# Kernel optimization log

Hardware: AMD Instinct MI355X
Metric: run time of the kernel (lower is better)

## Reference

```python
import jax, jax.numpy as jnp
import numpy as np

DIM = 192
T, H, W = 6, 8, 8
NH = 6
HD = DIM // NH
HW = H * W
N = T * HW
SCALE = HD ** (-0.5)
B_ = 128


def _sine_pos_enc():
    # Faithful port of get_sine_position_encoding(window_size[1:], dim // 2).
    npf = DIM // 2
    ones = jnp.ones((1, H, W), jnp.float32)
    y_embed = jnp.cumsum(ones, axis=1)
    x_embed = jnp.cumsum(ones, axis=2)
    two_pi = 2.0 * np.pi
    y_embed = y_embed / (y_embed[:, -1:, :] + 1e-6) * two_pi
    x_embed = x_embed / (x_embed[:, :, -1:] + 1e-6) * two_pi
    dim_t = jnp.arange(npf, dtype=jnp.float32)
    dim_t = 10000.0 ** (2.0 * jnp.floor(dim_t / 2.0) / npf)
    pos_x = x_embed[:, :, :, None] / dim_t
    pos_y = y_embed[:, :, :, None] / dim_t
    pos_x = jnp.stack((jnp.sin(pos_x[..., 0::2]), jnp.cos(pos_x[..., 1::2])), axis=4).reshape(1, H, W, npf)
    pos_y = jnp.stack((jnp.sin(pos_y[..., 0::2]), jnp.cos(pos_y[..., 1::2])), axis=4).reshape(1, H, W, npf)
    pos = jnp.concatenate((pos_y, pos_x), axis=3)  # (1, H, W, DIM)
    return pos.reshape(1, HW, DIM)


def setup_inputs() -> dict:
    key = jax.random.key(0)
    ks = jax.random.split(key, 6)
    s = 0.02
    return {
        "x": jax.random.normal(ks[0], (B_, N, DIM), jnp.float32),
        "Wqkv": jax.random.normal(ks[1], (3 * DIM, DIM), jnp.float32) * s,
        "Wproj": jax.random.normal(ks[2], (DIM, 2 * DIM), jnp.float32) * s,
        "bproj": jnp.zeros((DIM,), jnp.float32),
        "gamma": jnp.ones((DIM,), jnp.float32),
        "beta": jnp.zeros((DIM,), jnp.float32),
        "W1": jax.random.normal(ks[3], (DIM, DIM), jnp.float32) * s,
        "b1": jnp.zeros((DIM,), jnp.float32),
        "W2": jax.random.normal(ks[4], (DIM, DIM), jnp.float32) * s,
        "b2": jnp.zeros((DIM,), jnp.float32),
    }


def reference(x, Wqkv, Wproj, bproj, gamma, beta, W1, b1, W2, b2):
    b = x.shape[0]
    pos = jnp.tile(_sine_pos_enc(), (1, T, 1))  # (1, N, DIM)
    qkv = (x + pos) @ Wqkv.T                      # (b, N, 3*DIM)
    qkv = qkv.reshape(b, N, 3, NH, HD).transpose(2, 0, 3, 1, 4)
    # temporal chunks: (b, NH, T, HW, HD)
    q = qkv[0].reshape(b, NH, T, HW, HD)
    k = qkv[1].reshape(b, NH, T, HW, HD)
    v = qkv[2].reshape(b, NH, T, HW, HD)
    # all T x T cross-frame attention pairs at once
    scores = jnp.einsum('bhind,bhjmd->ijbhnm', q * SCALE, k)  # (T,T,b,NH,HW,HW)
    attn = jax.nn.softmax(scores, axis=-1)
    o = jnp.einsum('ijbhnm,bhjmd->ijbnhd', attn, v).reshape(T, T, b, HW, DIM)
    # Faithful to torch's x.view(-1, B_, HW, C): raw reinterpretation, not a transpose.
    x_tmp = x.reshape(T, b, HW, DIM)
    xi = jnp.broadcast_to(x_tmp[:, None], (T, T, b, HW, DIM))
    x_att = jnp.concatenate((o, xi), axis=-1)     # (T,T,b,HW,2*DIM)
    y = x_att @ Wproj.T + bproj
    mu = jnp.mean(y, axis=-1, keepdims=True)
    var = jnp.var(y, axis=-1, keepdims=True)
    y = (y - mu) / jnp.sqrt(var + 1e-5) * gamma + beta
    y = jax.nn.gelu(y @ W1.T + b1, approximate=False) @ W2.T + b2
    acc = jnp.sum(y, axis=1)                       # sum over j -> (T,b,HW,DIM)
    x_out = x + acc.transpose(1, 0, 2, 3).reshape(b, N, DIM) / T
    return jnp.concatenate((x, x_out), axis=-1)
```

## Files before the change

kernel.cpp:

```cpp
#include <hip/hip_runtime.h>
#include <cmath>

#define TT   6
#define NB   128
#define DIM  192
#define SCALE 0.17677669529663687f

typedef __attribute__((ext_vector_type(8))) short v8s;
typedef __attribute__((ext_vector_type(4))) float v4f;

__device__ __forceinline__ short f2bf(float f) {
  union { float f; unsigned u; } v; v.f = f;
  unsigned r = v.u + 0x7fffu + ((v.u >> 16) & 1u);
  return (short)(r >> 16);
}
__device__ __forceinline__ void fence() {
  __asm__ volatile("s_waitcnt lgkmcnt(0)" ::: "memory");
}

__global__ void cvt_kernel(const float* __restrict__ src, short* __restrict__ dst, int n4) {
  int idx = blockIdx.x * 256 + threadIdx.x;
  if (idx >= n4) return;
  const float* s = src + idx * 4;
  short4 r;
  r.x = f2bf(s[0]); r.y = f2bf(s[1]); r.z = f2bf(s[2]); r.w = f2bf(s[3]);
  *(short4*)(dst + idx * 4) = r;
}

__global__ void pos_kernel(float* __restrict__ pos) {
  int idx = blockIdx.x * 256 + threadIdx.x;
  if (idx >= 64 * 192) return;
  int row = idx / 192, c = idx - row * 192;
  int e  = (c < 96) ? (row >> 3) : (row & 7);
  int cc = (c < 96) ? c : c - 96;
  int m = cc >> 1;
  float embed = (float)(e + 1) * (6.283185307179586f / 8.000001f);
  float dt = powf(10000.0f, (float)m * (1.0f / 48.0f));
  float ang = embed / dt;
  pos[idx] = (cc & 1) ? cosf(ang) : sinf(ang);
}

__global__ __launch_bounds__(256) void qkv_kernel(
    const float* __restrict__ x, const float* __restrict__ pos,
    const short* __restrict__ Wqkv_bf,
    short* __restrict__ Qb, short* __restrict__ Kb, short* __restrict__ Vtb) {
  __shared__ short XP[64 * 200];
  int bid = blockIdx.x;
  int t = bid % TT, b = bid / TT;
  int tid = threadIdx.x, w = tid >> 6, lane = tid & 63;
  int l15 = lane & 15, quad = lane >> 4;
  const float* xrow = x + (size_t)(b * (TT * 64) + t * 64) * DIM;
  for (int c = tid; c < 64 * 24; c += 256) {
    int row = c / 24, col8 = (c - (c / 24) * 24) * 8;
    const float* xs = xrow + row * DIM + col8;
    const float* pp = pos + row * DIM + col8;
    v8s r8;
#pragma unroll
    for (int jj = 0; jj < 8; jj++) r8[jj] = f2bf(xs[jj] + pp[jj]);
    *(v8s*)(XP + row * 200 + col8) = r8;
  }
  __syncthreads();
  const v4f vzero = {0.f, 0.f, 0.f, 0.f};
  size_t obase = (size_t)(b * TT + t) * 64 * DIM;
#pragma unroll
  for (int cti = 0; cti < 9; cti++) {
    int r0 = w * 144 + cti * 16;
    v4f acc[4] = {vzero, vzero, vzero, vzero};
#pragma unroll
    for (int ks = 0; ks < 6; ks++) {
      v8s a = *(const v8s*)(Wqkv_bf + (size_t)(r0 + l15) * 192 + ks * 32 + quad * 8);
#pragma unroll
      for (int nt = 0; nt < 4; nt++) {
        v8s bb = *(const v8s*)(XP + (nt * 16 + l15) * 200 + ks * 32 + quad * 8);
        acc[nt] = __builtin_amdgcn_mfma_f32_16x16x32_bf16(a, bb, acc[nt], 0, 0, 0);
      }
    }
    int R = r0 + quad * 4;
#pragma unroll
    for (int nt = 0; nt < 4; nt++) {
      int hw = nt * 16 + l15;
      if (R < 192) {
        short4 s;
        s.x = f2bf(acc[nt][0] * SCALE); s.y = f2bf(acc[nt][1] * SCALE);
        s.z = f2bf(acc[nt][2] * SCALE); s.w = f2bf(acc[nt][3] * SCALE);
        *(short4*)(Qb + obase + (size_t)hw * 192 + R) = s;
      } else if (R < 384) {
        short4 s;
        s.x = f2bf(acc[nt][0]); s.y = f2bf(acc[nt][1]);
        s.z = f2bf(acc[nt][2]); s.w = f2bf(acc[nt][3]);
        *(short4*)(Kb + obase + (size_t)hw * 192 + (R - 192)) = s;
      } else {
#pragma unroll
        for (int r = 0; r < 4; r++)
          Vtb[obase + (size_t)(R - 384 + r) * 64 + hw] = f2bf(acc[nt][r]);
      }
    }
  }
}

__global__ __launch_bounds__(512, 4) void fused_all(
    const float* __restrict__ x,
    const short* __restrict__ Qb, const short* __restrict__ Kb,
    const short* __restrict__ Vtb,
    const short* __restrict__ Wproj_bf, const short* __restrict__ W1_bf,
    const short* __restrict__ W2_bf,
    const float* __restrict__ bproj, const float* __restrict__ gamma,
    const float* __restrict__ beta, const float* __restrict__ b1,
    const float* __restrict__ b2,
    float* __restrict__ out) {
  __shared__ short SP[64 * 200];
  __shared__ short Pl[8][16 * 72];
  __shared__ float LNp[64][4][2];

  int bid = blockIdx.x;
  int xcd = bid & 7, idx6 = bid >> 3;
  int bq = idx6 / TT;
  int b = xcd * 16 + bq, i = idx6 - bq * TT;

  int tid = threadIdx.x, w = tid >> 6, lane = tid & 63;
  int l15 = lane & 15, quad = lane >> 4;
  int wc = w & 3, wh = w >> 2;
  int cb = wc * 48;
  const v4f vzero = {0.f, 0.f, 0.f, 0.f};

  const float* xi = x + (size_t)(i * NB + b) * 64 * DIM;
  for (int c = tid; c < 64 * 24; c += 512) {
    int row = c / 24, col8 = (c - (c / 24) * 24) * 8;
    const float* xs = xi + row * DIM + col8;
    v8s r8;
#pragma unroll
    for (int jj = 0; jj < 8; jj++) r8[jj] = f2bf(xs[jj]);
    *(v8s*)(SP + row * 200 + col8) = r8;
  }
  __syncthreads();

  v4f y1x[3][2];
#pragma unroll
  for (int cti = 0; cti < 3; cti++)
#pragma unroll
    for (int nt = 0; nt < 2; nt++) y1x[cti][nt] = vzero;
#pragma unroll
  for (int ks = 0; ks < 6; ks++) {
    v8s bxi[2];
#pragma unroll
    for (int nt = 0; nt < 2; nt++)
      bxi[nt] = *(const v8s*)(SP + (wh * 32 + nt * 16 + l15) * 200 + ks * 32 + quad * 8);
#pragma unroll
    for (int cti = 0; cti < 3; cti++) {
      v8s a = *(const v8s*)(Wproj_bf + (size_t)(cb + cti * 16 + l15) * 384 + 192 + ks * 32 + quad * 8);
#pragma unroll
      for (int nt = 0; nt < 2; nt++)
        y1x[cti][nt] = __builtin_amdgcn_mfma_f32_16x16x32_bf16(a, bxi[nt], y1x[cti][nt], 0, 0, 0);
    }
  }

  v4f acc[3][2];
#pragma unroll
  for (int cti = 0; cti < 3; cti++)
#pragma unroll
    for (int nt = 0; nt < 2; nt++) acc[cti][nt] = vzero;

  const short* Qi = Qb + (size_t)(b * TT + i) * 64 * DIM;

  for (int j = 0; j < TT; j++) {
    __syncthreads();
    const short* Kj = Kb + (size_t)(b * TT + j) * 64 * DIM;
    const short* Vj = Vtb + (size_t)(b * TT + j) * 64 * DIM;

#pragma unroll
    for (int hh = 0; hh < 3; hh++) {
      int h = wh * 3 + hh;
      v8s qa = *(const v8s*)(Qi + (size_t)(wc * 16 + l15) * 192 + h * 32 + quad * 8);
      v4f S[4];
#pragma unroll
      for (int cta = 0; cta < 4; cta++) {
        v8s akq = *(const v8s*)(Kj + (size_t)(cta * 16 + l15) * 192 + h * 32 + quad * 8);
        S[cta] = __builtin_amdgcn_mfma_f32_16x16x32_bf16(akq, qa, vzero, 0, 0, 0);
      }
      float mx = -1e30f;
#pragma unroll
      for (int cta = 0; cta < 4; cta++)
#pragma unroll
        for (int r = 0; r < 4; r++) mx = fmaxf(mx, S[cta][r]);
      mx = fmaxf(mx, __shfl_xor(mx, 16, 64));
      mx = fmaxf(mx, __shfl_xor(mx, 32, 64));
      float sum = 0.f;
#pragma unroll
      for (int cta = 0; cta < 4; cta++)
#pragma unroll
        for (int r = 0; r < 4; r++) {
          float e = __expf(S[cta][r] - mx);
          S[cta][r] = e; sum += e;
        }
      sum += __shfl_xor(sum, 16, 64);
      sum += __shfl_xor(sum, 32, 64);
      float inv = 1.0f / sum;
#pragma unroll
      for (int cta = 0; cta < 4; cta++) {
        short4 s;
        s.x = f2bf(S[cta][0] * inv); s.y = f2bf(S[cta][1] * inv);
        s.z = f2bf(S[cta][2] * inv); s.w = f2bf(S[cta][3] * inv);
        *(short4*)(&Pl[w][l15 * 72 + cta * 16 + quad * 4]) = s;
      }
      fence();
      v8s bp0 = *(const v8s*)(&Pl[w][l15 * 72 + quad * 8]);
      v8s bp1 = *(const v8s*)(&Pl[w][l15 * 72 + 32 + quad * 8]);
#pragma unroll
      for (int ct2 = 0; ct2 < 2; ct2++) {
        v8s av0 = *(const v8s*)(Vj + (size_t)(h * 32 + ct2 * 16 + l15) * 64 + quad * 8);
        v8s av1 = *(const v8s*)(Vj + (size_t)(h * 32 + ct2 * 16 + l15) * 64 + 32 + quad * 8);
        v4f o = __builtin_amdgcn_mfma_f32_16x16x32_bf16(av0, bp0, vzero, 0, 0, 0);
        o = __builtin_amdgcn_mfma_f32_16x16x32_bf16(av1, bp1, o, 0, 0, 0);
        short4 s;
        s.x = f2bf(o[0]); s.y = f2bf(o[1]); s.z = f2bf(o[2]); s.w = f2bf(o[3]);
        *(short4*)(&SP[(wc * 16 + l15) * 200 + h * 32 + ct2 * 16 + quad * 4]) = s;
      }
      fence();
    }
    __syncthreads();

    v4f y1[3][2];
#pragma unroll
    for (int cti = 0; cti < 3; cti++)
#pragma unroll
      for (int nt = 0; nt < 2; nt++) y1[cti][nt] = y1x[cti][nt];
#pragma unroll
    for (int ks = 0; ks < 6; ks++) {
      v8s bo[2];
#pragma unroll
      for (int nt = 0; nt < 2; nt++)
        bo[nt] = *(const v8s*)(SP + (wh * 32 + nt * 16 + l15) * 200 + ks * 32 + quad * 8);
#pragma unroll
      for (int cti = 0; cti < 3; cti++) {
        v8s a = *(const v8s*)(Wproj_bf + (size_t)(cb + cti * 16 + l15) * 384 + ks * 32 + quad * 8);
#pragma unroll
        for (int nt = 0; nt < 2; nt++)
          y1[cti][nt] = __builtin_amdgcn_mfma_f32_16x16x32_bf16(a, bo[nt], y1[cti][nt], 0, 0, 0);
      }
    }
#pragma unroll
    for (int cti = 0; cti < 3; cti++) {
      float4 bp4 = *(const float4*)(bproj + cb + cti * 16 + quad * 4);
#pragma unroll
      for (int nt = 0; nt < 2; nt++) {
        y1[cti][nt][0] += bp4.x; y1[cti][nt][1] += bp4.y;
        y1[cti][nt][2] += bp4.z; y1[cti][nt][3] += bp4.w;
      }
    }
#pragma unroll
    for (int nt = 0; nt < 2; nt++) {
      float s1 = 0.f, s2 = 0.f;
#pragma unroll
      for (int cti = 0; cti < 3; cti++)
#pragma unroll
        for (int r = 0; r < 4; r++) { float v = y1[cti][nt][r]; s1 += v; s2 += v * v; }
      s1 += __shfl_xor(s1, 16, 64); s2 += __shfl_xor(s2, 16, 64);
      s1 += __shfl_xor(s1, 32, 64); s2 += __shfl_xor(s2, 32, 64);
      if (quad == 0) {
        LNp[wh * 32 + nt * 16 + l15][wc][0] = s1;
        LNp[wh * 32 + nt * 16 + l15][wc][1] = s2;
      }
    }
    __syncthreads();
    float mu[2], rs[2];
#pragma unroll
    for (int nt = 0; nt < 2; nt++) {
      int row = wh * 32 + nt * 16 + l15;
      float s1 = 0.f, s2 = 0.f;
#pragma unroll
      for (int ww = 0; ww < 4; ww++) { s1 += LNp[row][ww][0]; s2 += LNp[row][ww][1]; }
      float m = s1 * (1.0f / 192.0f);
      mu[nt] = m; rs[nt] = rsqrtf(s2 * (1.0f / 192.0f) - m * m + 1e-5f);
    }
#pragma unroll
    for (int cti = 0; cti < 3; cti++) {
      float4 g4 = *(const float4*)(gamma + cb + cti * 16 + quad * 4);
      float4 be4 = *(const float4*)(beta + cb + cti * 16 + quad * 4);
#pragma unroll
      for (int nt = 0; nt < 2; nt++) {
        short4 s;
        s.x = f2bf((y1[cti][nt][0] - mu[nt]) * rs[nt] * g4.x + be4.x);
        s.y = f2bf((y1[cti][nt][1] - mu[nt]) * rs[nt] * g4.y + be4.y);
        s.z = f2bf((y1[cti][nt][2] - mu[nt]) * rs[nt] * g4.z + be4.z);
        s.w = f2bf((y1[cti][nt][3] - mu[nt]) * rs[nt] * g4.w + be4.w);
        *(short4*)(&SP[(wh * 32 + nt * 16 + l15) * 200 + cb + cti * 16 + quad * 4]) = s;
      }
    }
    __syncthreads();

    v4f y2[3][2];
#pragma unroll
    for (int cti = 0; cti < 3; cti++)
#pragma unroll
      for (int nt = 0; nt < 2; nt++) y2[cti][nt] = vzero;
#pragma unroll
    for (int ks = 0; ks < 6; ks++) {
      v8s bh[2];
#pragma unroll
      for (int nt = 0; nt < 2; nt++)
        bh[nt] = *(const v8s*)(SP + (wh * 32 + nt * 16 + l15) * 200 + ks * 32 + quad * 8);
#pragma unroll
      for (int cti = 0; cti < 3; cti++) {
        v8s a = *(const v8s*)(W1_bf + (size_t)(cb + cti * 16 + l15) * 192 + ks * 32 + quad * 8);
#pragma unroll
        for (int nt = 0; nt < 2; nt++)
          y2[cti][nt] = __builtin_amdgcn_mfma_f32_16x16x32_bf16(a, bh[nt], y2[cti][nt], 0, 0, 0);
      }
    }
    __syncthreads();
#pragma unroll
    for (int cti = 0; cti < 3; cti++) {
      float4 b14 = *(const float4*)(b1 + cb + cti * 16 + quad * 4);
#pragma unroll
      for (int nt = 0; nt < 2; nt++) {
        float vv[4] = {y2[cti][nt][0] + b14.x, y2[cti][nt][1] + b14.y,
                       y2[cti][nt][2] + b14.z, y2[cti][nt][3] + b14.w};
        short sv[4];
#pragma unroll
        for (int r = 0; r < 4; r++) {
          float v = vv[r];
          float t = 0.79788456080286536f * (v + 0.044715f * v * v * v);
          float e = __expf(2.0f * t);
          float th = 1.0f - 2.0f / (e + 1.0f);
          sv[r] = f2bf(0.5f * v * (1.0f + th));
        }
        short4 s;
        s.x = sv[0]; s.y = sv[1]; s.z = sv[2]; s.w = sv[3];
        *(short4*)(&SP[(wh * 32 + nt * 16 + l15) * 200 + cb + cti * 16 + quad * 4]) = s;
      }
    }
    __syncthreads();

#pragma unroll
    for (int ks = 0; ks < 6; ks++) {
      v8s bh[2];
#pragma unroll
      for (int nt = 0; nt < 2; nt++)
        bh[nt] = *(const v8s*)(SP + (wh * 32 + nt * 16 + l15) * 200 + ks * 32 + quad * 8);
#pragma unroll
      for (int cti = 0; cti < 3; cti++) {
        v8s a = *(const v8s*)(W2_bf + (size_t)(cb + cti * 16 + l15) * 192 + ks * 32 + quad * 8);
#pragma unroll
        for (int nt = 0; nt < 2; nt++)
          acc[cti][nt] = __builtin_amdgcn_mfma_f32_16x16x32_bf16(a, bh[nt], acc[cti][nt], 0, 0, 0);
      }
    }
  }

#pragma unroll
  for (int cti = 0; cti < 3; cti++) {
    int cc0 = cb + cti * 16 + quad * 4;
    float4 b24 = *(const float4*)(b2 + cc0);
#pragma unroll
    for (int nt = 0; nt < 2; nt++) {
      int hw = wh * 32 + nt * 16 + l15;
      size_t nrow = (size_t)b * 384 + (size_t)i * 64 + hw;
      float4 xv = *(const float4*)(x + nrow * DIM + cc0);
      float4 o4;
      o4.x = xv.x + acc[cti][nt][0] * (1.0f / 6.0f) + b24.x;
      o4.y = xv.y + acc[cti][nt][1] * (1.0f / 6.0f) + b24.y;
      o4.z = xv.z + acc[cti][nt][2] * (1.0f / 6.0f) + b24.z;
      o4.w = xv.w + acc[cti][nt][3] * (1.0f / 6.0f) + b24.w;
      *(float4*)(out + nrow * 384 + 192 + cc0) = o4;
    }
  }
  for (int c = tid; c < 64 * 48; c += 512) {
    int row = c / 48, col4 = (c - (c / 48) * 48) * 4;
    size_t nrow = (size_t)b * 384 + (size_t)i * 64 + row;
    *(float4*)(out + nrow * 384 + col4) = *(const float4*)(x + nrow * DIM + col4);
  }
}

extern "C" void kernel_launch(void* const* d_in, const int* in_sizes, int n_in,
                              void* d_out, int out_size, void* d_ws, size_t ws_size,
                              hipStream_t stream) {
  (void)in_sizes; (void)n_in; (void)out_size; (void)ws_size;
  const float* x     = (const float*)d_in[0];
  const float* Wqkv  = (const float*)d_in[1];
  const float* Wproj = (const float*)d_in[2];
  const float* bproj = (const float*)d_in[3];
  const float* gamma = (const float*)d_in[4];
  const float* beta  = (const float*)d_in[5];
  const float* W1    = (const float*)d_in[6];
  const float* b1    = (const float*)d_in[7];
  const float* W2    = (const float*)d_in[8];
  const float* b2    = (const float*)d_in[9];
  float* out = (float*)d_out;

  short* Wqkv_bf  = (short*)d_ws;
  short* Wproj_bf = Wqkv_bf + 110592;
  short* W1_bf    = Wproj_bf + 73728;
  short* W2_bf    = W1_bf + 36864;
  float* pos_f    = (float*)(W2_bf + 36864);
  short* Qb       = (short*)(pos_f + 12288);
  short* Kb       = Qb + 9437184;
  short* Vtb      = Kb + 9437184;

  cvt_kernel<<<dim3(108), dim3(256), 0, stream>>>(Wqkv, Wqkv_bf, 110592 / 4);
  cvt_kernel<<<dim3(72), dim3(256), 0, stream>>>(Wproj, Wproj_bf, 73728 / 4);
  cvt_kernel<<<dim3(36), dim3(256), 0, stream>>>(W1, W1_bf, 36864 / 4);
  cvt_kernel<<<dim3(36), dim3(256), 0, stream>>>(W2, W2_bf, 36864 / 4);
  pos_kernel<<<dim3(48), dim3(256), 0, stream>>>(pos_f);
  qkv_kernel<<<dim3(TT * NB), dim3(256), 0, stream>>>(x, pos_f, Wqkv_bf, Qb, Kb, Vtb);
  fused_all<<<dim3(TT * NB), dim3(512), 0, stream>>>(
      x, Qb, Kb, Vtb, Wproj_bf, W1_bf, W2_bf, bproj, gamma, beta, b1, b2, out);
}
```

Baseline: 563.8 us.

## Merge prep kernels, shuffle P to registers, recompute x-proj per j, raise occupancy

Five small prep launches (four weight conversions and the position table) become one. In fused_all, the softmax probabilities are packed with v_cvt_pk_bf16_f32 and rearranged into the MFMA B-operand by cross-lane shuffles, replacing the per-wave LDS round-trip and its waitcnt fences. The x-projection is no longer kept in registers across the j loop but recomputed every iteration from a separate LDS copy of x. Q fragments are hoisted out of the j loop, and launch bounds rise to 6 blocks per CU. The aim is to cut register pressure and LDS traffic for more occupancy, at the cost of six times the x-projection MFMA work and more LDS per block, which may itself cap occupancy.

Result: slower. 637.4 us (+13.1%).

```diff
diff --git a/kernel.cpp b/kernel.cpp
--- a/kernel.cpp
+++ b/kernel.cpp
@@ -14,30 +14,41 @@
   unsigned r = v.u + 0x7fffu + ((v.u >> 16) & 1u);
   return (short)(r >> 16);
 }
-__device__ __forceinline__ void fence() {
-  __asm__ volatile("s_waitcnt lgkmcnt(0)" ::: "memory");
-}
-
-__global__ void cvt_kernel(const float* __restrict__ src, short* __restrict__ dst, int n4) {
+
+__global__ void prep_kernel(const float* __restrict__ Wqkv, const float* __restrict__ Wproj,
+                            const float* __restrict__ W1, const float* __restrict__ W2,
+                            short* __restrict__ dWqkv, short* __restrict__ dWproj,
+                            short* __restrict__ dW1, short* __restrict__ dW2,
+                            float* __restrict__ pos) {
   int idx = blockIdx.x * 256 + threadIdx.x;
-  if (idx >= n4) return;
-  const float* s = src + idx * 4;
+  const float* src = nullptr; short* dst = nullptr; int off = 0;
+  if (idx < 27648)      { src = Wqkv;  dst = dWqkv;  off = idx; }
+  else if (idx < 46080) { src = Wproj; dst = dWproj; off = idx - 27648; }
+  else if (idx < 55296) { src = W1;    dst = dW1;    off = idx - 46080; }
+  else if (idx < 64512) { src = W2;    dst = dW2;    off = idx - 55296; }
+  else if (idx < 67584) {
+    int p0 = (idx - 64512) * 4;
+    float4 r;
+    float* rp = (float*)&r;
+#pragma unroll
+    for (int jj = 0; jj < 4; jj++) {
+      int p = p0 + jj;
+      int row = p / 192, c = p - row * 192;
+      int e  = (c < 96) ? (row >> 3) : (row & 7);
+      int cc = (c < 96) ? c : c - 96;
+      int m = cc >> 1;
+      float embed = (float)(e + 1) * (6.283185307179586f / 8.000001f);
+      float dt = powf(10000.0f, (float)m * (1.0f / 48.0f));
+      float ang = embed / dt;
+      rp[jj] = (cc & 1) ? cosf(ang) : sinf(ang);
+    }
+    *(float4*)(pos + p0) = r;
+    return;
+  } else return;
+  const float* s = src + off * 4;
   short4 r;
   r.x = f2bf(s[0]); r.y = f2bf(s[1]); r.z = f2bf(s[2]); r.w = f2bf(s[3]);
-  *(short4*)(dst + idx * 4) = r;
-}
-
-__global__ void pos_kernel(float* __restrict__ pos) {
-  int idx = blockIdx.x * 256 + threadIdx.x;
-  if (idx >= 64 * 192) return;
-  int row = idx / 192, c = idx - row * 192;
-  int e  = (c < 96) ? (row >> 3) : (row & 7);
-  int cc = (c < 96) ? c : c - 96;
-  int m = cc >> 1;
-  float embed = (float)(e + 1) * (6.283185307179586f / 8.000001f);
-  float dt = powf(10000.0f, (float)m * (1.0f / 48.0f));
-  float ang = embed / dt;
-  pos[idx] = (cc & 1) ? cosf(ang) : sinf(ang);
+  *(short4*)(dst + off * 4) = r;
 }
 
 __global__ __launch_bounds__(256) void qkv_kernel(
@@ -98,7 +109,7 @@
   }
 }
 
-__global__ __launch_bounds__(512, 4) void fused_all(
+__global__ __launch_bounds__(512, 6) void fused_all(
     const float* __restrict__ x,
     const short* __restrict__ Qb, const short* __restrict__ Kb,
     const short* __restrict__ Vtb,
@@ -109,7 +120,7 @@
     const float* __restrict__ b2,
     float* __restrict__ out) {
   __shared__ short SP[64 * 200];
-  __shared__ short Pl[8][16 * 72];
+  __shared__ short XI[64 * 200];
   __shared__ float LNp[64][4][2];
 
   int bid = blockIdx.x;
@@ -130,37 +141,26 @@
     v8s r8;
 #pragma unroll
     for (int jj = 0; jj < 8; jj++) r8[jj] = f2bf(xs[jj]);
-    *(v8s*)(SP + row * 200 + col8) = r8;
-  }
+    *(v8s*)(XI + row * 200 + col8) = r8;
+  }
+
+  const short* Qi = Qb + (size_t)(b * TT + i) * 64 * DIM;
+  v8s qa[3];
+#pragma unroll
+  for (int hh = 0; hh < 3; hh++)
+    qa[hh] = *(const v8s*)(Qi + (size_t)(wc * 16 + l15) * 192 + (wh * 3 + hh) * 32 + quad * 8);
+
+  v4f acc[3][2];
+#pragma unroll
+  for (int cti = 0; cti < 3; cti++)
+#pragma unroll
+    for (int nt = 0; nt < 2; nt++) acc[cti][nt] = vzero;
+
   __syncthreads();
 
-  v4f y1x[3][2];
-#pragma unroll
-  for (int cti = 0; cti < 3; cti++)
-#pragma unroll
-    for (int nt = 0; nt < 2; nt++) y1x[cti][nt] = vzero;
-#pragma unroll
-  for (int ks = 0; ks < 6; ks++) {
-    v8s bxi[2];
-#pragma unroll
-    for (int nt = 0; nt < 2; nt++)
-      bxi[nt] = *(const v8s*)(SP + (wh * 32 + nt * 16 + l15) * 200 + ks * 32 + quad * 8);
-#pragma unroll
-    for (int cti = 0; cti < 3; cti++) {
-      v8s a = *(const v8s*)(Wproj_bf + (size_t)(cb + cti * 16 + l15) * 384 + 192 + ks * 32 + quad * 8);
-#pragma unroll
-      for (int nt = 0; nt < 2; nt++)
-        y1x[cti][nt] = __builtin_amdgcn_mfma_f32_16x16x32_bf16(a, bxi[nt], y1x[cti][nt], 0, 0, 0);
-    }
-  }
-
-  v4f acc[3][2];
-#pragma unroll
-  for (int cti = 0; cti < 3; cti++)
-#pragma unroll
-    for (int nt = 0; nt < 2; nt++) acc[cti][nt] = vzero;
-
-  const short* Qi = Qb + (size_t)(b * TT + i) * 64 * DIM;
+  int srcA = l15 + ((lane & 16) << 1);
+  int srcB = srcA + 16;
+  bool hiq = (lane & 32) != 0;
 
   for (int j = 0; j < TT; j++) {
     __syncthreads();
@@ -170,12 +170,11 @@
 #pragma unroll
     for (int hh = 0; hh < 3; hh++) {
       int h = wh * 3 + hh;
-      v8s qa = *(const v8s*)(Qi + (size_t)(wc * 16 + l15) * 192 + h * 32 + quad * 8);
       v4f S[4];
 #pragma unroll
       for (int cta = 0; cta < 4; cta++) {
         v8s akq = *(const v8s*)(Kj + (size_t)(cta * 16 + l15) * 192 + h * 32 + quad * 8);
-        S[cta] = __builtin_amdgcn_mfma_f32_16x16x32_bf16(akq, qa, vzero, 0, 0, 0);
+        S[cta] = __builtin_amdgcn_mfma_f32_16x16x32_bf16(akq, qa[hh], vzero, 0, 0, 0);
       }
       float mx = -1e30f;
 #pragma unroll
@@ -195,27 +194,37 @@
       sum += __shfl_xor(sum, 16, 64);
       sum += __shfl_xor(sum, 32, 64);
       float inv = 1.0f / sum;
+      unsigned pk[4][2];
 #pragma unroll
       for (int cta = 0; cta < 4; cta++) {
-        short4 s;
-        s.x = f2bf(S[cta][0] * inv); s.y = f2bf(S[cta][1] * inv);
-        s.z = f2bf(S[cta][2] * inv); s.w = f2bf(S[cta][3] * inv);
-        *(short4*)(&Pl[w][l15 * 72 + cta * 16 + quad * 4]) = s;
-      }
-      fence();
-      v8s bp0 = *(const v8s*)(&Pl[w][l15 * 72 + quad * 8]);
-      v8s bp1 = *(const v8s*)(&Pl[w][l15 * 72 + 32 + quad * 8]);
+        float a0 = S[cta][0] * inv, a1 = S[cta][1] * inv;
+        float a2 = S[cta][2] * inv, a3 = S[cta][3] * inv;
+        __asm__("v_cvt_pk_bf16_f32 %0, %1, %2" : "=v"(pk[cta][0]) : "v"(a0), "v"(a1));
+        __asm__("v_cvt_pk_bf16_f32 %0, %1, %2" : "=v"(pk[cta][1]) : "v"(a2), "v"(a3));
+      }
+      unsigned t00 = (unsigned)__shfl((int)pk[0][0], srcA), t10 = (unsigned)__shfl((int)pk[1][0], srcA);
+      unsigned t01 = (unsigned)__shfl((int)pk[0][1], srcA), t11 = (unsigned)__shfl((int)pk[1][1], srcA);
+      unsigned u00 = (unsigned)__shfl((int)pk[0][0], srcB), u10 = (unsigned)__shfl((int)pk[1][0], srcB);
+      unsigned u01 = (unsigned)__shfl((int)pk[0][1], srcB), u11 = (unsigned)__shfl((int)pk[1][1], srcB);
+      unsigned s20 = (unsigned)__shfl((int)pk[2][0], srcA), s30 = (unsigned)__shfl((int)pk[3][0], srcA);
+      unsigned s21 = (unsigned)__shfl((int)pk[2][1], srcA), s31 = (unsigned)__shfl((int)pk[3][1], srcA);
+      unsigned v20 = (unsigned)__shfl((int)pk[2][0], srcB), v30 = (unsigned)__shfl((int)pk[3][0], srcB);
+      unsigned v21 = (unsigned)__shfl((int)pk[2][1], srcB), v31 = (unsigned)__shfl((int)pk[3][1], srcB);
+      union { unsigned u[4]; v8s v; } B0, B1;
+      B0.u[0] = hiq ? t10 : t00;  B0.u[1] = hiq ? t11 : t01;
+      B0.u[2] = hiq ? u10 : u00;  B0.u[3] = hiq ? u11 : u01;
+      B1.u[0] = hiq ? s30 : s20;  B1.u[1] = hiq ? s31 : s21;
+      B1.u[2] = hiq ? v30 : v20;  B1.u[3] = hiq ? v31 : v21;
 #pragma unroll
       for (int ct2 = 0; ct2 < 2; ct2++) {
         v8s av0 = *(const v8s*)(Vj + (size_t)(h * 32 + ct2 * 16 + l15) * 64 + quad * 8);
         v8s av1 = *(const v8s*)(Vj + (size_t)(h * 32 + ct2 * 16 + l15) * 64 + 32 + quad * 8);
-        v4f o = __builtin_amdgcn_mfma_f32_16x16x32_bf16(av0, bp0, vzero, 0, 0, 0);
-        o = __builtin_amdgcn_mfma_f32_16x16x32_bf16(av1, bp1, o, 0, 0, 0);
+        v4f o = __builtin_amdgcn_mfma_f32_16x16x32_bf16(av0, B0.v, vzero, 0, 0, 0);
+        o = __builtin_amdgcn_mfma_f32_16x16x32_bf16(av1, B1.v, o, 0, 0, 0);
         short4 s;
         s.x = f2bf(o[0]); s.y = f2bf(o[1]); s.z = f2bf(o[2]); s.w = f2bf(o[3]);
         *(short4*)(&SP[(wc * 16 + l15) * 200 + h * 32 + ct2 * 16 + quad * 4]) = s;
       }
-      fence();
     }
     __syncthreads();
 
@@ -223,7 +232,7 @@
 #pragma unroll
     for (int cti = 0; cti < 3; cti++)
 #pragma unroll
-      for (int nt = 0; nt < 2; nt++) y1[cti][nt] = y1x[cti][nt];
+      for (int nt = 0; nt < 2; nt++) y1[cti][nt] = vzero;
 #pragma unroll
     for (int ks = 0; ks < 6; ks++) {
       v8s bo[2];
@@ -236,6 +245,20 @@
 #pragma unroll
         for (int nt = 0; nt < 2; nt++)
           y1[cti][nt] = __builtin_amdgcn_mfma_f32_16x16x32_bf16(a, bo[nt], y1[cti][nt], 0, 0, 0);
+      }
+    }
+#pragma unroll
+    for (int ks = 0; ks < 6; ks++) {
+      v8s bxi[2];
+#pragma unroll
+      for (int nt = 0; nt < 2; nt++)
+        bxi[nt] = *(const v8s*)(XI + (wh * 32 + nt * 16 + l15) * 200 + ks * 32 + quad * 8);
+#pragma unroll
+      for (int cti = 0; cti < 3; cti++) {
+        v8s a = *(const v8s*)(Wproj_bf + (size_t)(cb + cti * 16 + l15) * 384 + 192 + ks * 32 + quad * 8);
+#pragma unroll
+        for (int nt = 0; nt < 2; nt++)
+          y1[cti][nt] = __builtin_amdgcn_mfma_f32_16x16x32_bf16(a, bxi[nt], y1[cti][nt], 0, 0, 0);
       }
     }
 #pragma unroll
@@ -396,11 +419,8 @@
   short* Kb       = Qb + 9437184;
   short* Vtb      = Kb + 9437184;
 
-  cvt_kernel<<<dim3(108), dim3(256), 0, stream>>>(Wqkv, Wqkv_bf, 110592 / 4);
-  cvt_kernel<<<dim3(72), dim3(256), 0, stream>>>(Wproj, Wproj_bf, 73728 / 4);
-  cvt_kernel<<<dim3(36), dim3(256), 0, stream>>>(W1, W1_bf, 36864 / 4);
-  cvt_kernel<<<dim3(36), dim3(256), 0, stream>>>(W2, W2_bf, 36864 / 4);
-  pos_kernel<<<dim3(48), dim3(256), 0, stream>>>(pos_f);
+  prep_kernel<<<dim3(264), dim3(256), 0, stream>>>(
+      Wqkv, Wproj, W1, W2, Wqkv_bf, Wproj_bf, W1_bf, W2_bf, pos_f);
   qkv_kernel<<<dim3(TT * NB), dim3(256), 0, stream>>>(x, pos_f, Wqkv_bf, Qb, Kb, Vtb);
   fused_all<<<dim3(TT * NB), dim3(512), 0, stream>>>(
       x, Qb, Kb, Vtb, Wproj_bf, W1_bf, W2_bf, bproj, gamma, beta, b1, b2, out);
```
